# Kernel tuning notes

Measured on AMD Instinct MI355X. Metric: run time of the kernel, lower is better.

The kernel has to match this reference:

```python
import jax, jax.numpy as jnp
import numpy as np

B, T, EMB_D, HEAD = 8, 2048, 1024, 128


def setup_inputs() -> dict:
    key = jax.random.key(0)
    ks = jax.random.split(key, 7)
    s = 1.0 / np.sqrt(EMB_D)
    return {
        "inputs": jax.random.normal(ks[0], (B, T, EMB_D), dtype=jnp.float32),
        "Wk": jax.random.uniform(ks[1], (EMB_D, HEAD), jnp.float32, -s, s),
        "bk": jax.random.uniform(ks[2], (HEAD,), jnp.float32, -s, s),
        "Wq": jax.random.uniform(ks[3], (EMB_D, HEAD), jnp.float32, -s, s),
        "bq": jax.random.uniform(ks[4], (HEAD,), jnp.float32, -s, s),
        "Wv": jax.random.uniform(ks[5], (EMB_D, HEAD), jnp.float32, -s, s),
        "bv": jax.random.uniform(ks[6], (HEAD,), jnp.float32, -s, s),
    }


def reference(inputs, Wk, bk, Wq, bq, Wv, bv):
    # inputs: [B, T, C]
    Bq, Tq, _ = inputs.shape
    k = inputs @ Wk + bk  # [B, T, H]
    q = inputs @ Wq + bq
    v = inputs @ Wv + bv
    scale = HEAD ** -0.5
    weights = jnp.einsum("bth,bsh->bts", q, k) * scale  # [B, T, T]
    causal = jnp.tril(jnp.ones((Tq, Tq), dtype=bool))
    weights = jnp.where(causal, weights, -jnp.inf)
    # NOTE: original code applies softmax over dim=1 (the query axis), faithfully reproduced
    weights = jax.nn.softmax(weights, axis=1)
    return jnp.einsum("bts,bsh->bth", weights, v)  # [B, T, H]
```

## Files before the change

kernel.cpp:

```cpp
#include <hip/hip_runtime.h>
#include <hip/hip_bf16.h>

#define T_SEQ 2048
#define NBATCH 8
#define EMB 1024
#define HD 128

typedef _Float16 f16_t;
typedef _Float16 f16x8 __attribute__((ext_vector_type(8)));
typedef _Float16 f16x4 __attribute__((ext_vector_type(4)));
typedef float f32x4 __attribute__((ext_vector_type(4)));


__device__ __forceinline__ void g2l(const f16_t* g, f16_t* l) {
    __builtin_amdgcn_global_load_lds(
        (const __attribute__((address_space(1))) unsigned int*)g,
        (__attribute__((address_space(3))) unsigned int*)l, 16, 0, 0);
}

__global__ __launch_bounds__(256) void prep(
    const float* __restrict__ Wk, const float* __restrict__ bk,
    const float* __restrict__ Wq, const float* __restrict__ bq,
    const float* __restrict__ Wv, const float* __restrict__ bv,
    f16_t* __restrict__ w2, float* __restrict__ biasc,
    float4* __restrict__ out4, float4* __restrict__ colsum4) {
    int bid = blockIdx.x;
    int t = threadIdx.x;
    if (bid < 384) {
        int n = bid;
        const float scale = 0.08838834764831845f;
        const float* W; const float* bias; float sc; int col;
        if (n < 128)      { W = Wq; bias = bq; sc = scale; col = n; }
        else if (n < 256) { W = Wk; bias = bk; sc = 1.0f;  col = n - 128; }
        else              { W = Wv; bias = bv; sc = 1.0f;  col = n - 256; }
        if (t < 128) {
            int k0 = t * 8;
            f16x8 v;
            #pragma unroll
            for (int i = 0; i < 8; ++i) v[i] = (f16_t)(W[(size_t)(k0 + i) * HD + col] * sc);
            *(f16x8*)&w2[(size_t)(n >> 4) * 16384 + (size_t)(k0 >> 3) * 128 + (n & 15) * 8] = v;
        }
        if (t == 0) biasc[n] = bias[col] * sc;
    } else if (bid < 384 + 2048) {
        out4[(size_t)(bid - 384) * 256 + t] = make_float4(0.f, 0.f, 0.f, 0.f);
    } else {
        colsum4[(size_t)(bid - 2432) * 256 + t] = make_float4(0.f, 0.f, 0.f, 0.f);
    }
}

__global__ __launch_bounds__(256) void qkv_gemm(
    const float* __restrict__ X, const f16_t* __restrict__ w2,
    const float* __restrict__ biasc,
    f16_t* __restrict__ q2, f16_t* __restrict__ k2, f16_t* __restrict__ v2) {
    __shared__ f16_t Xs[64 * 72];

    int bid = blockIdx.x;
    int r8 = bid & 7, g = bid >> 3;
    int band = (g / 3) * 8 + r8;
    int i = g % 3;
    int m0 = band * 64, n0 = i * 128;
    int tid = threadIdx.x;
    int lane = tid & 63, w = tid >> 6;
    int quad = lane >> 4, l15 = lane & 15;
    int msub = (w & 1) * 32, nsub = (w >> 1) * 64;

    int srow = tid >> 2;
    int scg  = (tid & 3) * 16;

    const float* xrow = X + (size_t)(m0 + srow) * EMB + scg;

    f32x4 acc[2][4] = {};
    float4 pfA[4], pfB[4];
    #pragma unroll
    for (int u = 0; u < 4; ++u) pfA[u] = *(const float4*)(xrow + u * 4);
    #pragma unroll
    for (int u = 0; u < 4; ++u) pfB[u] = *(const float4*)(xrow + 64 + u * 4);

    auto stage = [&](float4 (&pf)[4]) {
        union { f16_t h[8]; uint4 u4; } p0, p1;
        p0.h[0] = (f16_t)pf[0].x; p0.h[1] = (f16_t)pf[0].y;
        p0.h[2] = (f16_t)pf[0].z; p0.h[3] = (f16_t)pf[0].w;
        p0.h[4] = (f16_t)pf[1].x; p0.h[5] = (f16_t)pf[1].y;
        p0.h[6] = (f16_t)pf[1].z; p0.h[7] = (f16_t)pf[1].w;
        p1.h[0] = (f16_t)pf[2].x; p1.h[1] = (f16_t)pf[2].y;
        p1.h[2] = (f16_t)pf[2].z; p1.h[3] = (f16_t)pf[2].w;
        p1.h[4] = (f16_t)pf[3].x; p1.h[5] = (f16_t)pf[3].y;
        p1.h[6] = (f16_t)pf[3].z; p1.h[7] = (f16_t)pf[3].w;
        *(uint4*)&Xs[srow * 72 + scg] = p0.u4;
        *(uint4*)&Xs[srow * 72 + scg + 8] = p1.u4;
    };
    auto compute = [&](int kc) {
        #pragma unroll
        for (int ks = 0; ks < 2; ++ks) {
            f16x8 afr0 = *(const f16x8*)&Xs[(msub + l15) * 72 + ks * 32 + quad * 8];
            f16x8 afr1 = *(const f16x8*)&Xs[(msub + 16 + l15) * 72 + ks * 32 + quad * 8];
            #pragma unroll
            for (int nf = 0; nf < 4; ++nf) {
                int ntile = (n0 + nsub + nf * 16) >> 4;
                f16x8 bfr = *(const f16x8*)&w2[(size_t)ntile * 16384 +
                    (size_t)((kc >> 3) + ks * 4 + quad) * 128 + l15 * 8];
                acc[0][nf] = __builtin_amdgcn_mfma_f32_16x16x32_f16(afr0, bfr, acc[0][nf], 0, 0, 0);
                acc[1][nf] = __builtin_amdgcn_mfma_f32_16x16x32_f16(afr1, bfr, acc[1][nf], 0, 0, 0);
            }
        }
    };

    for (int it = 0; it < 16; it += 2) {
        __syncthreads();
        stage(pfA);
        __syncthreads();
        if (it + 2 < 16) {
            #pragma unroll
            for (int u = 0; u < 4; ++u) pfA[u] = *(const float4*)(xrow + (it + 2) * 64 + u * 4);
        }
        compute(it * 64);

        __syncthreads();
        stage(pfB);
        __syncthreads();
        if (it + 3 < 16) {
            #pragma unroll
            for (int u = 0; u < 4; ++u) pfB[u] = *(const float4*)(xrow + (it + 3) * 64 + u * 4);
        }
        compute((it + 1) * 64);
    }

    #pragma unroll
    for (int nf = 0; nf < 4; ++nf) {
        int ng = n0 + nsub + nf * 16 + l15;
        float bval = biasc[ng];
        #pragma unroll
        for (int mf = 0; mf < 2; ++mf) {
            int rowg = m0 + msub + mf * 16 + quad * 4;
            f32x4 a = acc[mf][nf];
            if (ng < 256) {
                f16_t* dst = (ng < 128) ? q2 : k2;
                int c = ng & 127;
                #pragma unroll
                for (int r = 0; r < 4; ++r) {
                    int row = rowg + r;
                    dst[(size_t)(row >> 4) * 2048 + (c >> 3) * 128 + (row & 15) * 8 + (c & 7)]
                        = (f16_t)(a[r] + bval);
                }
            } else {
                int h = ng - 256;
                f16x4 hv;
                #pragma unroll
                for (int r = 0; r < 4; ++r) hv[r] = (f16_t)(a[r] + bval);
                *(f16x4*)&v2[(size_t)(rowg >> 3) * 1024 + h * 8 + (rowg & 7)] = hv;
            }
        }
    }
}

__global__ __launch_bounds__(256, 4) void col_stats(
    const f16_t* __restrict__ q2, const f16_t* __restrict__ k2,
    float* __restrict__ colsum) {
    __shared__ __align__(16) f16_t Ql[4 * 2048];

    int bid = blockIdx.x;
    int b = bid & 7;
    int item = 143 - (bid >> 3);
    int cg = 0, slab = 0, cum = 0;
    for (int c = 0; c < 32; ++c) {
        int n = (32 - c + 3) >> 2;
        if (item < cum + n) { cg = c; slab = item - cum; break; }
        cum += n;
    }
    int tc0 = cg + slab * 4, tc1 = min(tc0 + 4, 32);

    int tid = threadIdx.x, lane = tid & 63, w = tid >> 6;
    int quad = lane >> 4, l15 = lane & 15;
    int brow = b * 128;
    size_t base = (size_t)b * T_SEQ;

    f16x8 bfrs[4][4];
    #pragma unroll
    for (int st = 0; st < 4; ++st) {
        const f16_t* kt = k2 + (size_t)(brow + cg * 4 + st) * 2048 + l15 * 8;
        #pragma unroll
        for (int kf = 0; kf < 4; ++kf)
            bfrs[st][kf] = *(const f16x8*)(kt + (kf * 4 + quad) * 128);
    }

    float lacc[4] = {0.f, 0.f, 0.f, 0.f};

    for (int tc = tc0; tc < tc1; ++tc) {
        int tb = tc * 64;
        __syncthreads();
        const f16_t* qsrc = q2 + (size_t)(brow + tc * 4) * 2048;
        #pragma unroll
        for (int i = 0; i < 4; ++i)
            g2l(qsrc + i * 2048 + tid * 8, Ql + i * 2048 + tid * 8);
        __syncthreads();

        f16x8 afr[4];
        #pragma unroll
        for (int kf = 0; kf < 4; ++kf)
            afr[kf] = *(const f16x8*)&Ql[w * 2048 + (kf * 4 + quad) * 128 + l15 * 8];
        #pragma unroll
        for (int st = 0; st < 4; ++st) {
            f32x4 s = {};
            #pragma unroll
            for (int kf = 0; kf < 4; ++kf)
                s = __builtin_amdgcn_mfma_f32_16x16x32_f16(afr[kf], bfrs[st][kf], s, 0, 0, 0);
            int scol = cg * 64 + st * 16 + l15;
            #pragma unroll
            for (int r = 0; r < 4; ++r) {
                int t = tb + w * 16 + quad * 4 + r;
                if (t >= scol) lacc[st] += __expf(s[r]);
            }
        }
    }

    #pragma unroll
    for (int st = 0; st < 4; ++st) {
        float v = lacc[st];
        v += __shfl_xor(v, 16, 64);
        v += __shfl_xor(v, 32, 64);
        if (quad == 0) atomicAdd(&colsum[base + cg * 64 + st * 16 + l15], v);
    }
}

__global__ __launch_bounds__(256, 4) void attn_out(
    const f16_t* __restrict__ q2, const f16_t* __restrict__ k2,
    const f16_t* __restrict__ v2, const float* __restrict__ colsum,
    float* __restrict__ out) {
    __shared__ __align__(16) f16_t Kl[4 * 2048];
    __shared__ __align__(16) f16_t Vl[8 * 1024];
    __shared__ __align__(16) f16_t Pl[32 * 72];

    int bid = blockIdx.x;
    int b = bid & 7;
    int item = 159 - (bid >> 3);
    int g = 0, slab = 0, cum = 0;
    for (int gg = 0; gg < 64; ++gg) {
        int n = (((gg >> 1) + 1) + 7) >> 3;
        if (item < cum + n) { g = gg; slab = item - cum; break; }
        cum += n;
    }
    int nch = (g >> 1) + 1;
    int c0 = slab * 8, c1 = min(c0 + 8, nch);
    int trow = g * 32;

    int tid = threadIdx.x, lane = tid & 63, w = tid >> 6;
    int quad = lane >> 4, l15 = lane & 15;
    int brow = b * 128;
    size_t base = (size_t)b * T_SEQ;

    f16x8 qfr[2][4];
    #pragma unroll
    for (int tt = 0; tt < 2; ++tt) {
        const f16_t* qt = q2 + (size_t)(brow + 2 * g + tt) * 2048 + l15 * 8;
        #pragma unroll
        for (int kf = 0; kf < 4; ++kf)
            qfr[tt][kf] = *(const f16x8*)(qt + (kf * 4 + quad) * 128);
    }

    f32x4 o[2][2] = {};

    for (int c = c0; c < c1; ++c) {
        int sb = c * 64;
        __syncthreads();
        const f16_t* ksrc = k2 + (size_t)(brow + (sb >> 4)) * 2048;
        const f16_t* vsrc = v2 + (((size_t)base + sb) >> 3) * 1024;
        #pragma unroll
        for (int i = 0; i < 4; ++i) {
            g2l(ksrc + i * 2048 + tid * 8, Kl + i * 2048 + tid * 8);
            g2l(vsrc + i * 2048 + tid * 8, Vl + i * 2048 + tid * 8);
        }
        __syncthreads();

        float iv = 1.0f / colsum[base + sb + w * 16 + l15];
        int scol = sb + w * 16 + l15;
        f16x8 bfr[4];
        #pragma unroll
        for (int kf = 0; kf < 4; ++kf)
            bfr[kf] = *(const f16x8*)&Kl[w * 2048 + (kf * 4 + quad) * 128 + l15 * 8];
        #pragma unroll
        for (int tt = 0; tt < 2; ++tt) {
            f32x4 s = {};
            #pragma unroll
            for (int kf = 0; kf < 4; ++kf)
                s = __builtin_amdgcn_mfma_f32_16x16x32_f16(qfr[tt][kf], bfr[kf], s, 0, 0, 0);
            #pragma unroll
            for (int r = 0; r < 4; ++r) {
                int t = trow + tt * 16 + quad * 4 + r;
                float pv = (t >= scol) ? __expf(s[r]) * iv : 0.f;
                Pl[(tt * 16 + quad * 4 + r) * 72 + w * 16 + l15] = (f16_t)pv;
            }
        }
        __syncthreads();

        #pragma unroll
        for (int kf2 = 0; kf2 < 2; ++kf2) {
            f16x8 pa0 = *(const f16x8*)&Pl[(l15) * 72 + kf2 * 32 + quad * 8];
            f16x8 pa1 = *(const f16x8*)&Pl[(16 + l15) * 72 + kf2 * 32 + quad * 8];
            #pragma unroll
            for (int hh = 0; hh < 2; ++hh) {
                f16x8 vfr = *(const f16x8*)&Vl[(kf2 * 4 + quad) * 1024 + (w * 32 + hh * 16 + l15) * 8];
                o[0][hh] = __builtin_amdgcn_mfma_f32_16x16x32_f16(pa0, vfr, o[0][hh], 0, 0, 0);
                o[1][hh] = __builtin_amdgcn_mfma_f32_16x16x32_f16(pa1, vfr, o[1][hh], 0, 0, 0);
            }
        }
    }

    #pragma unroll
    for (int tt = 0; tt < 2; ++tt)
        #pragma unroll
        for (int hh = 0; hh < 2; ++hh)
            #pragma unroll
            for (int r = 0; r < 4; ++r)
                atomicAdd(&out[(base + trow + tt * 16 + quad * 4 + r) * HD + w * 32 + hh * 16 + l15],
                          o[tt][hh][r]);
}

extern "C" void kernel_launch(void* const* d_in, const int* in_sizes, int n_in,
                              void* d_out, int out_size, void* d_ws, size_t ws_size,
                              hipStream_t stream) {
    const float* X  = (const float*)d_in[0];
    const float* Wk = (const float*)d_in[1];
    const float* bk = (const float*)d_in[2];
    const float* Wq = (const float*)d_in[3];
    const float* bq = (const float*)d_in[4];
    const float* Wv = (const float*)d_in[5];
    const float* bv = (const float*)d_in[6];
    float* out = (float*)d_out;

    char* ws = (char*)d_ws;
    const size_t W2_B    = 24 * 16384 * 2;
    const size_t BIAS_B  = 2048;
    const size_t QKV_B   = (size_t)NBATCH * T_SEQ * HD * 2;
    f16_t* w2     = (f16_t*)ws;
    float* biasc  = (float*)(ws + W2_B);
    f16_t* q2     = (f16_t*)(ws + W2_B + BIAS_B);
    f16_t* k2     = (f16_t*)(ws + W2_B + BIAS_B + QKV_B);
    f16_t* v2     = (f16_t*)(ws + W2_B + BIAS_B + 2 * QKV_B);
    float* colsum = (float*)(ws + W2_B + BIAS_B + 3 * QKV_B);

    prep<<<dim3(2448), dim3(256), 0, stream>>>(Wk, bk, Wq, bq, Wv, bv, w2, biasc,
                                               (float4*)out, (float4*)colsum);
    qkv_gemm<<<dim3(768), dim3(256), 0, stream>>>(X, w2, biasc, q2, k2, v2);
    col_stats<<<dim3(1152), dim3(256), 0, stream>>>(q2, k2, colsum);
    attn_out<<<dim3(1280), dim3(256), 0, stream>>>(q2, k2, v2, colsum, out);
}
```

Before: 177.3 us.

## Rewrite QKV GEMM as per-wave 64x64 tiles loading operands directly from global

The QKV projection GEMM drops the shared-memory staging and block-level syncs. Each wave now computes its own 64x64 output tile, reading fp32 X rows directly from global memory, converting them to fp16 in registers, and reading weight fragments from global. The grid is halved and the waves are spread across XCDs through a bid remapping. This removes LDS traffic and barriers, but X loses reuse across waves, so more global and L2 traffic is possible and register pressure rises.

```diff
diff --git a/kernel.cpp b/kernel.cpp
--- a/kernel.cpp
+++ b/kernel.cpp
@@ -52,86 +52,68 @@
     const float* __restrict__ X, const f16_t* __restrict__ w2,
     const float* __restrict__ biasc,
     f16_t* __restrict__ q2, f16_t* __restrict__ k2, f16_t* __restrict__ v2) {
-    __shared__ f16_t Xs[64 * 72];
-
-    int bid = blockIdx.x;
-    int r8 = bid & 7, g = bid >> 3;
-    int band = (g / 3) * 8 + r8;
-    int i = g % 3;
-    int m0 = band * 64, n0 = i * 128;
     int tid = threadIdx.x;
     int lane = tid & 63, w = tid >> 6;
     int quad = lane >> 4, l15 = lane & 15;
-    int msub = (w & 1) * 32, nsub = (w >> 1) * 64;
-
-    int srow = tid >> 2;
-    int scg  = (tid & 3) * 16;
-
-    const float* xrow = X + (size_t)(m0 + srow) * EMB + scg;
-
-    f32x4 acc[2][4] = {};
-    float4 pfA[4], pfB[4];
-    #pragma unroll
-    for (int u = 0; u < 4; ++u) pfA[u] = *(const float4*)(xrow + u * 4);
-    #pragma unroll
-    for (int u = 0; u < 4; ++u) pfB[u] = *(const float4*)(xrow + 64 + u * 4);
-
-    auto stage = [&](float4 (&pf)[4]) {
-        union { f16_t h[8]; uint4 u4; } p0, p1;
-        p0.h[0] = (f16_t)pf[0].x; p0.h[1] = (f16_t)pf[0].y;
-        p0.h[2] = (f16_t)pf[0].z; p0.h[3] = (f16_t)pf[0].w;
-        p0.h[4] = (f16_t)pf[1].x; p0.h[5] = (f16_t)pf[1].y;
-        p0.h[6] = (f16_t)pf[1].z; p0.h[7] = (f16_t)pf[1].w;
-        p1.h[0] = (f16_t)pf[2].x; p1.h[1] = (f16_t)pf[2].y;
-        p1.h[2] = (f16_t)pf[2].z; p1.h[3] = (f16_t)pf[2].w;
-        p1.h[4] = (f16_t)pf[3].x; p1.h[5] = (f16_t)pf[3].y;
-        p1.h[6] = (f16_t)pf[3].z; p1.h[7] = (f16_t)pf[3].w;
-        *(uint4*)&Xs[srow * 72 + scg] = p0.u4;
-        *(uint4*)&Xs[srow * 72 + scg + 8] = p1.u4;
-    };
-    auto compute = [&](int kc) {
-        #pragma unroll
-        for (int ks = 0; ks < 2; ++ks) {
-            f16x8 afr0 = *(const f16x8*)&Xs[(msub + l15) * 72 + ks * 32 + quad * 8];
-            f16x8 afr1 = *(const f16x8*)&Xs[(msub + 16 + l15) * 72 + ks * 32 + quad * 8];
-            #pragma unroll
-            for (int nf = 0; nf < 4; ++nf) {
-                int ntile = (n0 + nsub + nf * 16) >> 4;
-                f16x8 bfr = *(const f16x8*)&w2[(size_t)ntile * 16384 +
-                    (size_t)((kc >> 3) + ks * 4 + quad) * 128 + l15 * 8];
-                acc[0][nf] = __builtin_amdgcn_mfma_f32_16x16x32_f16(afr0, bfr, acc[0][nf], 0, 0, 0);
-                acc[1][nf] = __builtin_amdgcn_mfma_f32_16x16x32_f16(afr1, bfr, acc[1][nf], 0, 0, 0);
-            }
-        }
-    };
-
-    for (int it = 0; it < 16; it += 2) {
-        __syncthreads();
-        stage(pfA);
-        __syncthreads();
-        if (it + 2 < 16) {
-            #pragma unroll
-            for (int u = 0; u < 4; ++u) pfA[u] = *(const float4*)(xrow + (it + 2) * 64 + u * 4);
-        }
-        compute(it * 64);
-
-        __syncthreads();
-        stage(pfB);
-        __syncthreads();
-        if (it + 3 < 16) {
-            #pragma unroll
-            for (int u = 0; u < 4; ++u) pfB[u] = *(const float4*)(xrow + (it + 3) * 64 + u * 4);
-        }
-        compute((it + 1) * 64);
+
+    int bid = blockIdx.x;
+    int g = (bid & 7) * 192 + (bid >> 3) * 4 + w;
+    int mt = g / 6, nt = g - mt * 6;
+    int m0 = mt * 64, n0 = nt * 64;
+
+    const float* arow = X + (size_t)(m0 + l15) * EMB + quad * 8;
+    const f16_t* bb = w2 + (size_t)(n0 >> 4) * 16384 + (size_t)quad * 128 + (size_t)l15 * 8;
+
+    f32x4 acc[4][4] = {};
+
+    for (int kc = 0; kc < 16; ++kc) {
+        float4 alo[4][2], ahi[4][2];
+        #pragma unroll
+        for (int mf = 0; mf < 4; ++mf) {
+            #pragma unroll
+            for (int ks = 0; ks < 2; ++ks) {
+                const float* p = arow + (size_t)mf * (16 * EMB) + kc * 64 + ks * 32;
+                alo[mf][ks] = *(const float4*)p;
+                ahi[mf][ks] = *(const float4*)(p + 4);
+            }
+        }
+        f16x8 bf[4][2];
+        #pragma unroll
+        for (int nf = 0; nf < 4; ++nf)
+            #pragma unroll
+            for (int ks = 0; ks < 2; ++ks)
+                bf[nf][ks] = *(const f16x8*)(bb + (size_t)nf * 16384 +
+                                             (size_t)(kc * 8 + ks * 4) * 128);
+        f16x8 af[4][2];
+        #pragma unroll
+        for (int mf = 0; mf < 4; ++mf) {
+            #pragma unroll
+            for (int ks = 0; ks < 2; ++ks) {
+                f16x8 v;
+                v[0] = (f16_t)alo[mf][ks].x; v[1] = (f16_t)alo[mf][ks].y;
+                v[2] = (f16_t)alo[mf][ks].z; v[3] = (f16_t)alo[mf][ks].w;
+                v[4] = (f16_t)ahi[mf][ks].x; v[5] = (f16_t)ahi[mf][ks].y;
+                v[6] = (f16_t)ahi[mf][ks].z; v[7] = (f16_t)ahi[mf][ks].w;
+                af[mf][ks] = v;
+            }
+        }
+        #pragma unroll
+        for (int ks = 0; ks < 2; ++ks)
+            #pragma unroll
+            for (int mf = 0; mf < 4; ++mf)
+                #pragma unroll
+                for (int nf = 0; nf < 4; ++nf)
+                    acc[mf][nf] = __builtin_amdgcn_mfma_f32_16x16x32_f16(
+                        af[mf][ks], bf[nf][ks], acc[mf][nf], 0, 0, 0);
     }
 
     #pragma unroll
     for (int nf = 0; nf < 4; ++nf) {
-        int ng = n0 + nsub + nf * 16 + l15;
+        int ng = n0 + nf * 16 + l15;
         float bval = biasc[ng];
         #pragma unroll
-        for (int mf = 0; mf < 2; ++mf) {
-            int rowg = m0 + msub + mf * 16 + quad * 4;
+        for (int mf = 0; mf < 4; ++mf) {
+            int rowg = m0 + mf * 16 + quad * 4;
             f32x4 a = acc[mf][nf];
             if (ng < 256) {
                 f16_t* dst = (ng < 128) ? q2 : k2;
@@ -340,7 +322,7 @@
 
     prep<<<dim3(2448), dim3(256), 0, stream>>>(Wk, bk, Wq, bq, Wv, bv, w2, biasc,
                                                (float4*)out, (float4*)colsum);
-    qkv_gemm<<<dim3(768), dim3(256), 0, stream>>>(X, w2, biasc, q2, k2, v2);
+    qkv_gemm<<<dim3(384), dim3(256), 0, stream>>>(X, w2, biasc, q2, k2, v2);
     col_stats<<<dim3(1152), dim3(256), 0, stream>>>(q2, k2, colsum);
     attn_out<<<dim3(1280), dim3(256), 0, stream>>>(q2, k2, v2, colsum, out);
 }
```

After: 216.3 us. 22.0% more time.

## Stage QKV weight tiles in LDS via async loads with double-buffered pipeline

Applied to the files above, without the earlier changes.

The QKV projection GEMM now copies each weight chunk into shared memory with global_load_lds instead of having every wave read weight fragments straight from global memory. Both the X tile and the weight tile are double-buffered, so the next chunk's loads overlap the current chunk's MFMAs, and the loop needs one barrier per chunk instead of four per two chunks. This raises LDS use to about 50KB per block, which may lower occupancy. There is no explicit wait on the async LDS loads other than the barrier, so correctness depends on the compiler inserting the vmcnt wait.

```diff
diff --git a/kernel.cpp b/kernel.cpp
--- a/kernel.cpp
+++ b/kernel.cpp
@@ -52,7 +52,8 @@
     const float* __restrict__ X, const f16_t* __restrict__ w2,
     const float* __restrict__ biasc,
     f16_t* __restrict__ q2, f16_t* __restrict__ k2, f16_t* __restrict__ v2) {
-    __shared__ f16_t Xs[64 * 72];
+    __shared__ f16_t Xs[2][64 * 72];
+    __shared__ __align__(16) f16_t Bl[2][8 * 1024];
 
     int bid = blockIdx.x;
     int r8 = bid & 7, g = bid >> 3;
@@ -68,15 +69,25 @@
     int scg  = (tid & 3) * 16;
 
     const float* xrow = X + (size_t)(m0 + srow) * EMB + scg;
+    const f16_t* bbase = w2 + (size_t)(n0 >> 4) * 16384;
 
     f32x4 acc[2][4] = {};
-    float4 pfA[4], pfB[4];
-    #pragma unroll
-    for (int u = 0; u < 4; ++u) pfA[u] = *(const float4*)(xrow + u * 4);
-    #pragma unroll
-    for (int u = 0; u < 4; ++u) pfB[u] = *(const float4*)(xrow + 64 + u * 4);
-
-    auto stage = [&](float4 (&pf)[4]) {
+    float4 pf[4];
+
+    auto loadA = [&](int kc) {
+        #pragma unroll
+        for (int u = 0; u < 4; ++u) pf[u] = *(const float4*)(xrow + kc * 64 + u * 4);
+    };
+    auto stageB = [&](int kc, int buf) {
+        const f16_t* bsrc = bbase + (size_t)kc * 1024;
+        #pragma unroll
+        for (int ii = 0; ii < 4; ++ii) {
+            int D = tid * 16 + ii * 4096;
+            g2l(bsrc + (size_t)(D >> 11) * 16384 + ((D & 2047) >> 1),
+                &Bl[buf][D >> 1]);
+        }
+    };
+    auto stageA = [&](int buf) {
         union { f16_t h[8]; uint4 u4; } p0, p1;
         p0.h[0] = (f16_t)pf[0].x; p0.h[1] = (f16_t)pf[0].y;
         p0.h[2] = (f16_t)pf[0].z; p0.h[3] = (f16_t)pf[0].w;
@@ -86,43 +97,38 @@
         p1.h[2] = (f16_t)pf[2].z; p1.h[3] = (f16_t)pf[2].w;
         p1.h[4] = (f16_t)pf[3].x; p1.h[5] = (f16_t)pf[3].y;
         p1.h[6] = (f16_t)pf[3].z; p1.h[7] = (f16_t)pf[3].w;
-        *(uint4*)&Xs[srow * 72 + scg] = p0.u4;
-        *(uint4*)&Xs[srow * 72 + scg + 8] = p1.u4;
+        *(uint4*)&Xs[buf][srow * 72 + scg] = p0.u4;
+        *(uint4*)&Xs[buf][srow * 72 + scg + 8] = p1.u4;
     };
-    auto compute = [&](int kc) {
+    auto compute = [&](int buf) {
         #pragma unroll
         for (int ks = 0; ks < 2; ++ks) {
-            f16x8 afr0 = *(const f16x8*)&Xs[(msub + l15) * 72 + ks * 32 + quad * 8];
-            f16x8 afr1 = *(const f16x8*)&Xs[(msub + 16 + l15) * 72 + ks * 32 + quad * 8];
+            f16x8 afr0 = *(const f16x8*)&Xs[buf][(msub + l15) * 72 + ks * 32 + quad * 8];
+            f16x8 afr1 = *(const f16x8*)&Xs[buf][(msub + 16 + l15) * 72 + ks * 32 + quad * 8];
             #pragma unroll
             for (int nf = 0; nf < 4; ++nf) {
-                int ntile = (n0 + nsub + nf * 16) >> 4;
-                f16x8 bfr = *(const f16x8*)&w2[(size_t)ntile * 16384 +
-                    (size_t)((kc >> 3) + ks * 4 + quad) * 128 + l15 * 8];
+                int ntl = (nsub >> 4) + nf;
+                f16x8 bfr = *(const f16x8*)&Bl[buf][ntl * 1024 + (ks * 4 + quad) * 128 + l15 * 8];
                 acc[0][nf] = __builtin_amdgcn_mfma_f32_16x16x32_f16(afr0, bfr, acc[0][nf], 0, 0, 0);
                 acc[1][nf] = __builtin_amdgcn_mfma_f32_16x16x32_f16(afr1, bfr, acc[1][nf], 0, 0, 0);
             }
         }
     };
 
-    for (int it = 0; it < 16; it += 2) {
-        __syncthreads();
-        stage(pfA);
-        __syncthreads();
-        if (it + 2 < 16) {
-            #pragma unroll
-            for (int u = 0; u < 4; ++u) pfA[u] = *(const float4*)(xrow + (it + 2) * 64 + u * 4);
-        }
-        compute(it * 64);
-
-        __syncthreads();
-        stage(pfB);
-        __syncthreads();
-        if (it + 3 < 16) {
-            #pragma unroll
-            for (int u = 0; u < 4; ++u) pfB[u] = *(const float4*)(xrow + (it + 3) * 64 + u * 4);
-        }
-        compute((it + 1) * 64);
+    loadA(0);
+    stageB(0, 0);
+    stageA(0);
+    __syncthreads();
+
+    for (int kc = 0; kc < 16; ++kc) {
+        int cur = kc & 1, nxt = cur ^ 1;
+        if (kc + 1 < 16) {
+            loadA(kc + 1);
+            stageB(kc + 1, nxt);
+        }
+        compute(cur);
+        if (kc + 1 < 16) stageA(nxt);
+        __syncthreads();
     }
 
     #pragma unroll
```

Result: no change. 174.4 us (-1.6%).
